# Kernel optimization log

Measured on AMD Instinct MI355X. Metric: run time of the kernel, lower is better.

Reference implementation:

```python
import jax, jax.numpy as jnp
import numpy as np

N_NODES = 100000
N_EDGES = 1600000
IN_C, HID_C, OUT_C = 128, 128, 64


def setup_inputs() -> dict:
    key = jax.random.key(0)
    ks = jax.random.split(key, 9)
    features = jax.random.normal(ks[0], (N_NODES, IN_C), dtype=jnp.float32)
    src = jax.random.randint(ks[1], (N_EDGES,), 0, N_NODES, dtype=jnp.int32)
    dst = jax.random.randint(ks[2], (N_EDGES,), 0, N_NODES, dtype=jnp.int32)
    def glorot(k, fan_in, fan_out):
        lim = float(np.sqrt(6.0 / (fan_in + fan_out)))
        return jax.random.uniform(k, (fan_in, fan_out), jnp.float32, -lim, lim)
    return {
        "features": features, "src": src, "dst": dst,
        "W1": glorot(ks[3], IN_C, HID_C), "b1": jnp.zeros((HID_C,), jnp.float32),
        "W2": glorot(ks[4], HID_C, HID_C), "b2": jnp.zeros((HID_C,), jnp.float32),
        "W3": glorot(ks[5], HID_C, OUT_C), "b3": jnp.zeros((OUT_C,), jnp.float32),
    }


def _graph_conv(x, src, dst, W, b, inv_sqrt_out, inv_sqrt_in):
    # DGL GraphConv, norm='both': h = D_in^{-1/2} A D_out^{-1/2} (x W) + b
    h = (x * inv_sqrt_out[:, None]) @ W            # [N, out]
    agg = jax.ops.segment_sum(h[src], dst, num_segments=N_NODES)
    return agg * inv_sqrt_in[:, None] + b


def reference(features, src, dst, W1, b1, W2, b2, W3, b3):
    ones = jnp.ones((N_EDGES,), jnp.float32)
    deg_out = jnp.clip(jax.ops.segment_sum(ones, src, num_segments=N_NODES), 1.0)
    deg_in = jnp.clip(jax.ops.segment_sum(ones, dst, num_segments=N_NODES), 1.0)
    iso, isi = deg_out ** -0.5, deg_in ** -0.5
    x = jax.nn.relu(_graph_conv(features, src, dst, W1, b1, iso, isi))
    x = jax.nn.relu(_graph_conv(x, src, dst, W2, b2, iso, isi))
    x = _graph_conv(x, src, dst, W3, b3, iso, isi)
    return jax.nn.log_softmax(x, axis=1)
```

## Files before the change

kernel.cpp:

```cpp
#include <hip/hip_runtime.h>
#include <hip/hip_bf16.h>

#define IN_C 128
#define HID_C 128
#define OUT_C 64

typedef unsigned short u16;
typedef unsigned int   u32;
typedef __attribute__((ext_vector_type(8))) short short8;
typedef __attribute__((ext_vector_type(4))) float f32x4;
typedef __attribute__((ext_vector_type(2))) float f32x2;

__device__ __forceinline__ u16 bf16_bits(float x) {
    __hip_bfloat16 h = __float2bfloat16(x);
    return *(u16*)&h;
}
__device__ __forceinline__ void split_hi_lo(float a, u16& hi, u16& lo) {
    __hip_bfloat16 h = __float2bfloat16(a);
    float hf = __bfloat162float(h);
    __hip_bfloat16 l = __float2bfloat16(a - hf);
    hi = *(u16*)&h; lo = *(u16*)&l;
}
__device__ __forceinline__ void pk_acc(f32x2& acc, u32 v) {
    f32x2 val;
    val.x = __uint_as_float(v << 16);
    val.y = __uint_as_float(v & 0xffff0000u);
    asm("v_pk_add_f32 %0, %0, %1" : "+v"(acc) : "v"(val));
}


__global__ __launch_bounds__(256)
void part_hist2(const int* __restrict__ src, const int* __restrict__ dst,
                int* __restrict__ bh, int E, int K, int NB) {
    const int b = blockIdx.x;
    extern __shared__ int lh[];
    for (int i = threadIdx.x; i < 2 * K; i += 256) lh[i] = 0;
    __syncthreads();
    const int lo = (int)((long long)E * b / NB);
    const int hi = (int)((long long)E * (b + 1) / NB);
    for (int i = lo + threadIdx.x; i < hi; i += 256) {
        int d = __builtin_nontemporal_load(&dst[i]);
        int s = __builtin_nontemporal_load(&src[i]);
        atomicAdd(&lh[d >> 8], 1);
        atomicAdd(&lh[K + (s >> 8)], 1);
    }
    __syncthreads();
    for (int k = threadIdx.x; k < K; k += 256) {
        bh[k * NB + b]            = lh[k];
        bh[(K + k) * NB + b]      = lh[K + k];
    }
}

__global__ __launch_bounds__(256)
void part_scatter2(const int* __restrict__ src, const int* __restrict__ dst,
                   const int* __restrict__ ofs, u32* __restrict__ pairs,
                   int E, int K, int NB) {
    const int b = blockIdx.x;
    extern __shared__ int lcur[];
    for (int k = threadIdx.x; k < 2 * K; k += 256) lcur[k] = ofs[k * NB + b];
    __syncthreads();
    const int lo = (int)((long long)E * b / NB);
    const int hi = (int)((long long)E * (b + 1) / NB);
    for (int i = lo + threadIdx.x; i < hi; i += 256) {
        int d = __builtin_nontemporal_load(&dst[i]);
        int s = __builtin_nontemporal_load(&src[i]);
        int p1 = atomicAdd(&lcur[d >> 8], 1);
        pairs[p1] = ((u32)s << 8) | (u32)(d & 255);
        int p2 = atomicAdd(&lcur[K + (s >> 8)], 1);
        pairs[p2] = (u32)s;
    }
}

__global__ __launch_bounds__(256)
void bucket_count2(const u32* __restrict__ pairs, const int* __restrict__ OFS,
                   int* __restrict__ cnt_in, int* __restrict__ cnt_out,
                   int N, int NB, int K, int E) {
    const int kk = blockIdx.x;
    const bool is_src = kk >= K;
    const int k = is_src ? kk - K : kk;
    const int* ofs = OFS + (is_src ? K * NB : 0);
    int* cnt = is_src ? cnt_out : cnt_in;
    const int cap = is_src ? 2 * E : E;
    __shared__ int lc[256];
    lc[threadIdx.x] = 0;
    __syncthreads();
    const int s0 = ofs[k * NB];
    const int s1 = (k == K - 1) ? cap : ofs[(k + 1) * NB];
    for (int i = s0 + threadIdx.x; i < s1; i += 256)
        atomicAdd(&lc[pairs[i] & 255], 1);
    __syncthreads();
    const int node = k * 256 + threadIdx.x;
    if (node < N) cnt[node] = lc[threadIdx.x];
}

__global__ __launch_bounds__(256)
void bucket_fill(const u32* __restrict__ pairs, const int* __restrict__ ofs,
                 const int* __restrict__ row_start, int* __restrict__ csr,
                 int N, int NB, int K, int E) {
    const int k = blockIdx.x;
    __shared__ int lcur[256];
    const int node = k * 256 + threadIdx.x;
    lcur[threadIdx.x] = (node < N) ? row_start[node] : 0;
    __syncthreads();
    const int s0 = ofs[k * NB];
    const int s1 = (k == K - 1) ? E : ofs[(k + 1) * NB];
    for (int i = s0 + threadIdx.x; i < s1; i += 256) {
        u32 pr = pairs[i];
        int p = atomicAdd(&lcur[pr & 255], 1);
        csr[p] = (int)(pr >> 8);
    }
    __syncthreads();
    if (node < N) {
        int end = row_start[node + 1];
        for (int q = lcur[threadIdx.x]; q < end; ++q) csr[q] = N;
    }
}


__global__ __launch_bounds__(256)
void scan_pass1(const int* __restrict__ in, int* __restrict__ blocksum, int M) {
    const int b = blockIdx.x, t = threadIdx.x;
    const int base = b * 1024 + t * 4;
    int s = 0;
#pragma unroll
    for (int j = 0; j < 4; ++j) {
        int idx = base + j;
        if (idx < M) s += in[idx];
    }
#pragma unroll
    for (int off = 32; off >= 1; off >>= 1) s += __shfl_xor(s, off);
    __shared__ int wsum[4];
    if ((t & 63) == 0) wsum[t >> 6] = s;
    __syncthreads();
    if (t == 0) blocksum[b] = wsum[0] + wsum[1] + wsum[2] + wsum[3];
}

__global__ __launch_bounds__(256)
void scan_pass1p(const int* __restrict__ in, int* __restrict__ blocksum, int M) {
    const int b = blockIdx.x, t = threadIdx.x;
    const int base = b * 1024 + t * 4;
    int s = 0;
#pragma unroll
    for (int j = 0; j < 4; ++j) {
        int idx = base + j;
        if (idx < M) s += (in[idx] + 3) & ~3;
    }
#pragma unroll
    for (int off = 32; off >= 1; off >>= 1) s += __shfl_xor(s, off);
    __shared__ int wsum[4];
    if ((t & 63) == 0) wsum[t >> 6] = s;
    __syncthreads();
    if (t == 0) blocksum[b] = wsum[0] + wsum[1] + wsum[2] + wsum[3];
}

__global__ __launch_bounds__(1024)
void scan_g2(int* __restrict__ a, int nb) {
    __shared__ int s[1024];
    const int t = threadIdx.x;
    int v = (t < nb) ? a[t] : 0;
    s[t] = v;
    __syncthreads();
    for (int off = 1; off < 1024; off <<= 1) {
        int x = (t >= off) ? s[t - off] : 0;
        __syncthreads();
        s[t] += x;
        __syncthreads();
    }
    if (t < nb) a[t] = s[t] - v;
}

__global__ __launch_bounds__(256)
void scan_g3(const int* __restrict__ in, const int* __restrict__ blockoff,
             int* __restrict__ out, int M) {
    __shared__ int ssum[256];
    const int b = blockIdx.x, t = threadIdx.x;
    const int base = b * 1024 + t * 4;
    int c[4];
#pragma unroll
    for (int j = 0; j < 4; ++j) {
        int idx = base + j;
        c[j] = (idx < M) ? in[idx] : 0;
    }
    const int tot = c[0] + c[1] + c[2] + c[3];
    ssum[t] = tot;
    __syncthreads();
    for (int off = 1; off < 256; off <<= 1) {
        int v = (t >= off) ? ssum[t - off] : 0;
        __syncthreads();
        ssum[t] += v;
        __syncthreads();
    }
    int run = blockoff[b] + ssum[t] - tot;
#pragma unroll
    for (int j = 0; j < 4; ++j) {
        int idx = base + j;
        if (idx < M) { out[idx] = run; run += c[j]; }
    }
}

__global__ __launch_bounds__(256)
void scan_pass3n(const int* __restrict__ cnt_in, const int* __restrict__ cnt_out,
                 const int* __restrict__ blockoff, int* __restrict__ row_start,
                 float* __restrict__ iso, float* __restrict__ isi, int N) {
    __shared__ int ssum[256];
    const int b = blockIdx.x, t = threadIdx.x;
    const int base = b * 1024 + t * 4;
    int c[4];
#pragma unroll
    for (int j = 0; j < 4; ++j) {
        int idx = base + j;
        c[j] = (idx < N) ? cnt_in[idx] : 0;
    }
    const int tot = ((c[0] + 3) & ~3) + ((c[1] + 3) & ~3) + ((c[2] + 3) & ~3) + ((c[3] + 3) & ~3);
    ssum[t] = tot;
    __syncthreads();
    for (int off = 1; off < 256; off <<= 1) {
        int v = (t >= off) ? ssum[t - off] : 0;
        __syncthreads();
        ssum[t] += v;
        __syncthreads();
    }
    int run = blockoff[b] + ssum[t] - tot;
#pragma unroll
    for (int j = 0; j < 4; ++j) {
        int idx = base + j;
        if (idx < N) {
            row_start[idx] = run;
            run += (c[j] + 3) & ~3;
            int di = c[j] < 1 ? 1 : c[j];
            int co = cnt_out[idx];
            int dd = co < 1 ? 1 : co;
            isi[idx] = rsqrtf((float)di);
            iso[idx] = rsqrtf((float)dd);
            if (idx == N - 1) row_start[N] = run;
        }
    }
}


__global__ __launch_bounds__(128)
void wt_prep_all(const float* __restrict__ W1, const float* __restrict__ W2,
                 const float* __restrict__ W3, u16* __restrict__ Wt1,
                 u16* __restrict__ Wt2, u16* __restrict__ Wt3) {
    const int b = blockIdx.x, k = threadIdx.x;
    if (b < 128)       Wt1[b * 128 + k] = bf16_bits(W1[k * 128 + b]);
    else if (b < 256)  { int c = b - 128; Wt2[c * 128 + k] = bf16_bits(W2[k * 128 + c]); }
    else               { int c = b - 256; Wt3[c * 128 + k] = bf16_bits(W3[k * 64 + c]); }
}


template <int C>
__device__ __forceinline__
void mfma_store2(const u16* sAh, const u16* sAl, const u16* __restrict__ Wt,
                 u16* __restrict__ H, int row0, int N, int t) {
    constexpr int NT = C / 16;
    const int wid = t >> 6, lane = t & 63;
    const int r0 = wid * 16;
    const int arow = r0 + (lane & 15);
    const int kb = (lane >> 4) * 8;

    f32x4 acc[NT];
#pragma unroll
    for (int i = 0; i < NT; ++i) acc[i] = (f32x4){0.f, 0.f, 0.f, 0.f};

    const u16* wbase = Wt + (size_t)(lane & 15) * 128 + kb;

#pragma unroll
    for (int kk = 0; kk < 4; ++kk) {
        short8 ah = *(const short8*)(&sAh[arow * 136 + kk * 32 + kb]);
        short8 al = *(const short8*)(&sAl[arow * 136 + kk * 32 + kb]);
#pragma unroll
        for (int ct = 0; ct < NT; ++ct) {
            short8 bf = *(const short8*)(wbase + ct * 16 * 128 + kk * 32);
            acc[ct] = __builtin_amdgcn_mfma_f32_16x16x32_bf16(ah, bf, acc[ct], 0, 0, 0);
            acc[ct] = __builtin_amdgcn_mfma_f32_16x16x32_bf16(al, bf, acc[ct], 0, 0, 0);
        }
    }

    const int rbase = row0 + r0 + (lane >> 4) * 4;
#pragma unroll
    for (int ct = 0; ct < NT; ++ct) {
        int gcol = ct * 16 + (lane & 15);
#pragma unroll
        for (int r = 0; r < 4; ++r) {
            int grow = rbase + r;
            if (grow < N) H[(size_t)grow * C + gcol] = bf16_bits(acc[ct][r]);
        }
    }
}

template <int C>
__device__ __forceinline__
void mfma_store1(const u16* sA, const u16* __restrict__ Wt,
                 u16* __restrict__ H, int row0, int N, int t) {
    constexpr int NT = C / 16;
    const int wid = t >> 6, lane = t & 63;
    const int r0 = wid * 16;
    const int arow = r0 + (lane & 15);
    const int kb = (lane >> 4) * 8;

    f32x4 acc[NT];
#pragma unroll
    for (int i = 0; i < NT; ++i) acc[i] = (f32x4){0.f, 0.f, 0.f, 0.f};

    const u16* wbase = Wt + (size_t)(lane & 15) * 128 + kb;

#pragma unroll
    for (int kk = 0; kk < 4; ++kk) {
        short8 a = *(const short8*)(&sA[arow * 136 + kk * 32 + kb]);
#pragma unroll
        for (int ct = 0; ct < NT; ++ct) {
            short8 bf = *(const short8*)(wbase + ct * 16 * 128 + kk * 32);
            acc[ct] = __builtin_amdgcn_mfma_f32_16x16x32_bf16(a, bf, acc[ct], 0, 0, 0);
        }
    }

    const int rbase = row0 + r0 + (lane >> 4) * 4;
#pragma unroll
    for (int ct = 0; ct < NT; ++ct) {
        int gcol = ct * 16 + (lane & 15);
#pragma unroll
        for (int r = 0; r < 4; ++r) {
            int grow = rbase + r;
            if (grow < N) H[(size_t)grow * C + gcol] = bf16_bits(acc[ct][r]);
        }
    }
}


__global__ __launch_bounds__(256)
void gemm1_fused(const float* __restrict__ X, const float* __restrict__ iso,
                 const u16* __restrict__ Wt, u16* __restrict__ H, int N) {
    __shared__ u16 sAh[64 * 136];
    __shared__ u16 sAl[64 * 136];
    const int t = threadIdx.x;
    const int row0 = blockIdx.x * 64;

    if (blockIdx.x == 0 && t < 64) ((u32*)H)[(size_t)N * 64 + t] = 0;

    for (int i = t; i < 2048; i += 256) {
        int r = i >> 5, kv = (i & 31) << 2;
        int gr = row0 + r;
        if (gr >= N) gr = N - 1;
        float s = iso[gr];
        float4 x = *(const float4*)(X + (size_t)gr * 128 + kv);
        u16 h0, l0, h1, l1, h2, l2, h3, l3;
        split_hi_lo(x.x * s, h0, l0);
        split_hi_lo(x.y * s, h1, l1);
        split_hi_lo(x.z * s, h2, l2);
        split_hi_lo(x.w * s, h3, l3);
        uint2 hp = make_uint2((u32)h0 | ((u32)h1 << 16), (u32)h2 | ((u32)h3 << 16));
        uint2 lp = make_uint2((u32)l0 | ((u32)l1 << 16), (u32)l2 | ((u32)l3 << 16));
        *(uint2*)(&sAh[r * 136 + kv]) = hp;
        *(uint2*)(&sAl[r * 136 + kv]) = lp;
    }
    __syncthreads();
    mfma_store2<128>(sAh, sAl, Wt, H, row0, N, t);
}


template <int C>
__global__ __launch_bounds__(256)
void gemm_mfma(const u16* __restrict__ A,
               const u16* __restrict__ Wt, u16* __restrict__ H, int N) {
    __shared__ u16 sA[64 * 136];
    const int t = threadIdx.x;
    const int row0 = blockIdx.x * 64;

    if (blockIdx.x == 0 && t < C / 2) ((u32*)H)[(size_t)N * (C / 2) + t] = 0;

    for (int c = t; c < 1024; c += 256) {
        int r = c >> 4, kc = c & 15;
        int gr = row0 + r;
        if (gr >= N) gr = N - 1;
        *(uint4*)(&sA[r * 136 + kc * 8]) = *(const uint4*)(A + (size_t)gr * 128 + kc * 8);
    }
    __syncthreads();
    mfma_store1<C>(sA, Wt, H, row0, N, t);
}


__device__ __forceinline__
void gather128w(const u16* __restrict__ Hin, const int* __restrict__ csr,
                int rs, int re, int lane, f32x2* acc) {
    const int sub = lane >> 4;
    const int cb  = (lane & 15) * 8;
    int e = rs;
    while (e < re) {
        int nloc = re - e;
        if (nloc > 64) nloc = 64;
        int idx = (lane < nloc) ? __builtin_nontemporal_load(&csr[e + lane]) : 0;
        int j = 0;
        for (; j + 16 <= nloc; j += 16) {
            int r0 = __shfl(idx, j + sub);
            int r1 = __shfl(idx, j + 4 + sub);
            int r2 = __shfl(idx, j + 8 + sub);
            int r3 = __shfl(idx, j + 12 + sub);
            uint4 v0 = *(const uint4*)(Hin + (size_t)r0 * 128 + cb);
            uint4 v1 = *(const uint4*)(Hin + (size_t)r1 * 128 + cb);
            uint4 v2 = *(const uint4*)(Hin + (size_t)r2 * 128 + cb);
            uint4 v3 = *(const uint4*)(Hin + (size_t)r3 * 128 + cb);
            pk_acc(acc[0], v0.x); pk_acc(acc[1], v0.y); pk_acc(acc[2], v0.z); pk_acc(acc[3], v0.w);
            pk_acc(acc[0], v1.x); pk_acc(acc[1], v1.y); pk_acc(acc[2], v1.z); pk_acc(acc[3], v1.w);
            pk_acc(acc[0], v2.x); pk_acc(acc[1], v2.y); pk_acc(acc[2], v2.z); pk_acc(acc[3], v2.w);
            pk_acc(acc[0], v3.x); pk_acc(acc[1], v3.y); pk_acc(acc[2], v3.z); pk_acc(acc[3], v3.w);
        }
        for (; j < nloc; j += 4) {
            int r0 = __shfl(idx, j + sub);
            uint4 v0 = *(const uint4*)(Hin + (size_t)r0 * 128 + cb);
            pk_acc(acc[0], v0.x); pk_acc(acc[1], v0.y); pk_acc(acc[2], v0.z); pk_acc(acc[3], v0.w);
        }
        e += nloc;
    }
}


__global__ __launch_bounds__(256)
void agg_relu(const u16* __restrict__ H, const int* __restrict__ row_start,
              const int* __restrict__ csr_src, const float* __restrict__ isi,
              const float* __restrict__ iso, const float* __restrict__ bias,
              u16* __restrict__ A, int N) {
    const int wid  = (int)((blockIdx.x * (size_t)blockDim.x + threadIdx.x) >> 6);
    const int lane = threadIdx.x & 63;
    if (wid >= N) return;
    const int rs = row_start[wid];
    const int re = row_start[wid + 1];

    f32x2 acc[4];
#pragma unroll
    for (int i = 0; i < 4; ++i) { acc[i].x = 0.f; acc[i].y = 0.f; }
    gather128w(H, csr_src, rs, re, lane, acc);

#pragma unroll
    for (int i = 0; i < 4; ++i) {
        acc[i].x += __shfl_xor(acc[i].x, 16); acc[i].y += __shfl_xor(acc[i].y, 16);
        acc[i].x += __shfl_xor(acc[i].x, 32); acc[i].y += __shfl_xor(acc[i].y, 32);
    }

    if (lane < 16) {
        const float sc = isi[wid], so = iso[wid];
        float4 ba = *(const float4*)(bias + lane * 8);
        float4 bb = *(const float4*)(bias + lane * 8 + 4);
        float o[8];
        o[0] = acc[0].x * sc + ba.x; o[1] = acc[0].y * sc + ba.y;
        o[2] = acc[1].x * sc + ba.z; o[3] = acc[1].y * sc + ba.w;
        o[4] = acc[2].x * sc + bb.x; o[5] = acc[2].y * sc + bb.y;
        o[6] = acc[3].x * sc + bb.z; o[7] = acc[3].y * sc + bb.w;
        u32 hp[4];
#pragma unroll
        for (int i = 0; i < 4; ++i) {
            u16 h0 = bf16_bits(fmaxf(o[2 * i], 0.f) * so);
            u16 h1 = bf16_bits(fmaxf(o[2 * i + 1], 0.f) * so);
            hp[i] = (u32)h0 | ((u32)h1 << 16);
        }
        *(uint4*)(A + (size_t)wid * 128 + lane * 8) = *(uint4*)hp;
    }
}


__global__ __launch_bounds__(256)
void agg_final(const u16* __restrict__ H, const int* __restrict__ row_start,
               const int* __restrict__ csr_src, const float* __restrict__ isi,
               const float* __restrict__ bias, float* __restrict__ Out, int N) {
    const int wid  = (int)((blockIdx.x * (size_t)blockDim.x + threadIdx.x) >> 6);
    const int lane = threadIdx.x & 63;
    if (wid >= N) return;
    const int rs = row_start[wid];
    const int re = row_start[wid + 1];
    const int sub = lane >> 4;
    const int cb  = (lane & 15) * 4;

    f32x2 a0, a1;
    a0.x = a0.y = a1.x = a1.y = 0.f;
    int e = rs;
    while (e < re) {
        int nloc = re - e;
        if (nloc > 64) nloc = 64;
        int idx = (lane < nloc) ? __builtin_nontemporal_load(&csr_src[e + lane]) : 0;
        int j = 0;
        for (; j + 16 <= nloc; j += 16) {
            int r0 = __shfl(idx, j + sub);
            int r1 = __shfl(idx, j + 4 + sub);
            int r2 = __shfl(idx, j + 8 + sub);
            int r3 = __shfl(idx, j + 12 + sub);
            uint2 v0 = *(const uint2*)(H + (size_t)r0 * 64 + cb);
            uint2 v1 = *(const uint2*)(H + (size_t)r1 * 64 + cb);
            uint2 v2 = *(const uint2*)(H + (size_t)r2 * 64 + cb);
            uint2 v3 = *(const uint2*)(H + (size_t)r3 * 64 + cb);
            pk_acc(a0, v0.x); pk_acc(a1, v0.y);
            pk_acc(a0, v1.x); pk_acc(a1, v1.y);
            pk_acc(a0, v2.x); pk_acc(a1, v2.y);
            pk_acc(a0, v3.x); pk_acc(a1, v3.y);
        }
        for (; j < nloc; j += 4) {
            int r0 = __shfl(idx, j + sub);
            uint2 v0 = *(const uint2*)(H + (size_t)r0 * 64 + cb);
            pk_acc(a0, v0.x); pk_acc(a1, v0.y);
        }
        e += nloc;
    }

    a0.x += __shfl_xor(a0.x, 16); a0.y += __shfl_xor(a0.y, 16);
    a0.x += __shfl_xor(a0.x, 32); a0.y += __shfl_xor(a0.y, 32);
    a1.x += __shfl_xor(a1.x, 16); a1.y += __shfl_xor(a1.y, 16);
    a1.x += __shfl_xor(a1.x, 32); a1.y += __shfl_xor(a1.y, 32);

    const float sc = isi[wid];
    float4 b4 = *(const float4*)(bias + (lane & 15) * 4);
    float v0 = a0.x * sc + b4.x;
    float v1 = a0.y * sc + b4.y;
    float v2 = a1.x * sc + b4.z;
    float v3 = a1.y * sc + b4.w;
    float m = fmaxf(fmaxf(v0, v1), fmaxf(v2, v3));
#pragma unroll
    for (int off = 8; off >= 1; off >>= 1) m = fmaxf(m, __shfl_xor(m, off));
    float ss = expf(v0 - m) + expf(v1 - m) + expf(v2 - m) + expf(v3 - m);
#pragma unroll
    for (int off = 8; off >= 1; off >>= 1) ss += __shfl_xor(ss, off);
    float lg = m + logf(ss);
    if (lane < 16) {
        float4 o = make_float4(v0 - lg, v1 - lg, v2 - lg, v3 - lg);
        *(float4*)(Out + (size_t)wid * 64 + lane * 4) = o;
    }
}


extern "C" void kernel_launch(void* const* d_in, const int* in_sizes, int n_in,
                              void* d_out, int out_size, void* d_ws, size_t ws_size,
                              hipStream_t stream) {
    const float* features = (const float*)d_in[0];
    const int*   src      = (const int*)d_in[1];
    const int*   dst      = (const int*)d_in[2];
    const float* W1       = (const float*)d_in[3];
    const float* b1       = (const float*)d_in[4];
    const float* W2       = (const float*)d_in[5];
    const float* b2       = (const float*)d_in[6];
    const float* W3       = (const float*)d_in[7];
    const float* b3       = (const float*)d_in[8];
    float*       out      = (float*)d_out;

    const int N  = in_sizes[0] / IN_C;
    const int E  = in_sizes[1];
    const int K  = (N + 255) >> 8;
    const int NB = 256;
    const int M  = 2 * K * NB;
    const int nbe = (M + 1023) / 1024;
    const int nb  = (N + 1023) / 1024;

    char* ws = (char*)d_ws;
    const size_t SLOT = 400128;
    int*   cnt_out   = (int*)(ws + 0 * SLOT);
    int*   cnt_in    = (int*)(ws + 1 * SLOT);
    int*   row_start = (int*)(ws + 2 * SLOT);
    float* iso       = (float*)(ws + 3 * SLOT);
    float* isi       = (float*)(ws + 4 * SLOT);
    int*   blocksum  = (int*)(ws + 5 * SLOT);
    int*   eblocksum = blocksum + 2048;
    int*   csr       = (int*)(ws + 6 * SLOT);
    char*  p         = ws + 6 * SLOT + 8000000;
    int*   BH        = (int*)p;
    int*   OFS       = (int*)(p + 1000000);
    u32*   pairs     = (u32*)(p + 2000000);
    u16*   Hb        = (u16*)(p + 14800000);
    u16*   Ab        = (u16*)(p + 40500000);
    u16*   Wt1       = (u16*)(p + 66100000);
    u16*   Wt2       = Wt1 + 128 * 128;
    u16*   Wt3       = Wt2 + 128 * 128;

    const size_t ldsK2 = (size_t)(2 * K) * sizeof(int);

    part_hist2<<<NB, 256, ldsK2, stream>>>(src, dst, BH, E, K, NB);
    scan_pass1<<<nbe, 256, 0, stream>>>(BH, eblocksum, M);
    scan_g2<<<1, 1024, 0, stream>>>(eblocksum, nbe);
    scan_g3<<<nbe, 256, 0, stream>>>(BH, eblocksum, OFS, M);
    part_scatter2<<<NB, 256, ldsK2, stream>>>(src, dst, OFS, pairs, E, K, NB);
    bucket_count2<<<2 * K, 256, 0, stream>>>(pairs, OFS, cnt_in, cnt_out, N, NB, K, E);
    scan_pass1p<<<nb, 256, 0, stream>>>(cnt_in, blocksum, N);
    scan_g2<<<1, 1024, 0, stream>>>(blocksum, nb);
    scan_pass3n<<<nb, 256, 0, stream>>>(cnt_in, cnt_out, blocksum, row_start, iso, isi, N);
    bucket_fill<<<K, 256, 0, stream>>>(pairs, OFS, row_start, csr, N, NB, K, E);

    wt_prep_all<<<320, 128, 0, stream>>>(W1, W2, W3, Wt1, Wt2, Wt3);

    const int gblocks = (N + 63) / 64;
    const int ablocks = (int)(((size_t)N * 64 + 255) / 256);

    gemm1_fused<<<gblocks, 256, 0, stream>>>(features, iso, Wt1, Hb, N);
    agg_relu<<<ablocks, 256, 0, stream>>>(Hb, row_start, csr, isi, iso, b1, Ab, N);
    gemm_mfma<128><<<gblocks, 256, 0, stream>>>(Ab, Wt2, Hb, N);
    agg_relu<<<ablocks, 256, 0, stream>>>(Hb, row_start, csr, isi, iso, b2, Ab, N);
    gemm_mfma<64><<<gblocks, 256, 0, stream>>>(Ab, Wt3, Hb, N);
    agg_final<<<ablocks, 256, 0, stream>>>(Hb, row_start, csr, isi, b3, out, N);
}
```

Measured before the change: 358.6 us.

## Compute out-degree via global atomics and fuse per-bucket count, scan and CSR fill

The source-side partition (second histogram and scatter of src pairs) is replaced by a direct global-atomic out-degree count. In-degree counting, the padded row-offset scan, the normalization factors and the CSR fill are merged into one per-bucket kernel. Row offsets now come from the bucket offset plus a per-bucket local scan with padding slack (k*768), so aggregation kernels take an explicit row_end array. This cuts several launches and halves the pair traffic, at the cost of global atomic contention on the out-degree counters and gaps in the CSR layout.

```diff
diff --git a/kernel.cpp b/kernel.cpp
--- a/kernel.cpp
+++ b/kernel.cpp
@@ -29,90 +29,100 @@
 }
 
 
-__global__ __launch_bounds__(256)
-void part_hist2(const int* __restrict__ src, const int* __restrict__ dst,
-                int* __restrict__ bh, int E, int K, int NB) {
+__global__ void zero_kernel(int* __restrict__ p, int n) {
+    int i = blockIdx.x * blockDim.x + threadIdx.x;
+    if (i < n) p[i] = 0;
+}
+
+__global__ void degree_src(const int* __restrict__ src, int* __restrict__ cnt, int E) {
+    for (int i = blockIdx.x * blockDim.x + threadIdx.x; i < E; i += gridDim.x * blockDim.x)
+        atomicAdd(&cnt[src[i]], 1);
+}
+
+
+__global__ __launch_bounds__(256)
+void part_hist(const int* __restrict__ dst, int* __restrict__ bh,
+               int E, int K, int NB) {
     const int b = blockIdx.x;
     extern __shared__ int lh[];
-    for (int i = threadIdx.x; i < 2 * K; i += 256) lh[i] = 0;
+    for (int i = threadIdx.x; i < K; i += 256) lh[i] = 0;
+    __syncthreads();
+    const int lo = (int)((long long)E * b / NB);
+    const int hi = (int)((long long)E * (b + 1) / NB);
+    for (int i = lo + threadIdx.x; i < hi; i += 256)
+        atomicAdd(&lh[__builtin_nontemporal_load(&dst[i]) >> 8], 1);
+    __syncthreads();
+    for (int k = threadIdx.x; k < K; k += 256)
+        bh[k * NB + b] = lh[k];
+}
+
+__global__ __launch_bounds__(256)
+void part_scatter(const int* __restrict__ src, const int* __restrict__ dst,
+                  const int* __restrict__ ofs, u32* __restrict__ pairs,
+                  int E, int K, int NB) {
+    const int b = blockIdx.x;
+    extern __shared__ int lcur[];
+    for (int k = threadIdx.x; k < K; k += 256) lcur[k] = ofs[k * NB + b];
     __syncthreads();
     const int lo = (int)((long long)E * b / NB);
     const int hi = (int)((long long)E * (b + 1) / NB);
     for (int i = lo + threadIdx.x; i < hi; i += 256) {
         int d = __builtin_nontemporal_load(&dst[i]);
         int s = __builtin_nontemporal_load(&src[i]);
-        atomicAdd(&lh[d >> 8], 1);
-        atomicAdd(&lh[K + (s >> 8)], 1);
-    }
-    __syncthreads();
-    for (int k = threadIdx.x; k < K; k += 256) {
-        bh[k * NB + b]            = lh[k];
-        bh[(K + k) * NB + b]      = lh[K + k];
-    }
-}
-
-__global__ __launch_bounds__(256)
-void part_scatter2(const int* __restrict__ src, const int* __restrict__ dst,
-                   const int* __restrict__ ofs, u32* __restrict__ pairs,
-                   int E, int K, int NB) {
-    const int b = blockIdx.x;
-    extern __shared__ int lcur[];
-    for (int k = threadIdx.x; k < 2 * K; k += 256) lcur[k] = ofs[k * NB + b];
-    __syncthreads();
-    const int lo = (int)((long long)E * b / NB);
-    const int hi = (int)((long long)E * (b + 1) / NB);
-    for (int i = lo + threadIdx.x; i < hi; i += 256) {
-        int d = __builtin_nontemporal_load(&dst[i]);
-        int s = __builtin_nontemporal_load(&src[i]);
-        int p1 = atomicAdd(&lcur[d >> 8], 1);
-        pairs[p1] = ((u32)s << 8) | (u32)(d & 255);
-        int p2 = atomicAdd(&lcur[K + (s >> 8)], 1);
-        pairs[p2] = (u32)s;
-    }
-}
-
-__global__ __launch_bounds__(256)
-void bucket_count2(const u32* __restrict__ pairs, const int* __restrict__ OFS,
-                   int* __restrict__ cnt_in, int* __restrict__ cnt_out,
-                   int N, int NB, int K, int E) {
-    const int kk = blockIdx.x;
-    const bool is_src = kk >= K;
-    const int k = is_src ? kk - K : kk;
-    const int* ofs = OFS + (is_src ? K * NB : 0);
-    int* cnt = is_src ? cnt_out : cnt_in;
-    const int cap = is_src ? 2 * E : E;
+        int p = atomicAdd(&lcur[d >> 8], 1);
+        pairs[p] = ((u32)s << 8) | (u32)(d & 255);
+    }
+}
+
+__global__ __launch_bounds__(256)
+void bucket_count_fill(const u32* __restrict__ pairs, const int* __restrict__ OFS,
+                       const int* __restrict__ cnt_out,
+                       int* __restrict__ csr, int* __restrict__ row_start,
+                       int* __restrict__ row_end, float* __restrict__ iso,
+                       float* __restrict__ isi, int N, int NB, int K, int E) {
+    const int k = blockIdx.x, t = threadIdx.x;
     __shared__ int lc[256];
-    lc[threadIdx.x] = 0;
-    __syncthreads();
-    const int s0 = ofs[k * NB];
-    const int s1 = (k == K - 1) ? cap : ofs[(k + 1) * NB];
-    for (int i = s0 + threadIdx.x; i < s1; i += 256)
+    __shared__ int lpre[256];
+    lc[t] = 0;
+    __syncthreads();
+    const int s0 = OFS[k * NB];
+    const int s1 = (k == K - 1) ? E : OFS[(k + 1) * NB];
+    for (int i = s0 + t; i < s1; i += 256)
         atomicAdd(&lc[pairs[i] & 255], 1);
     __syncthreads();
-    const int node = k * 256 + threadIdx.x;
-    if (node < N) cnt[node] = lc[threadIdx.x];
-}
-
-__global__ __launch_bounds__(256)
-void bucket_fill(const u32* __restrict__ pairs, const int* __restrict__ ofs,
-                 const int* __restrict__ row_start, int* __restrict__ csr,
-                 int N, int NB, int K, int E) {
-    const int k = blockIdx.x;
-    __shared__ int lcur[256];
-    const int node = k * 256 + threadIdx.x;
-    lcur[threadIdx.x] = (node < N) ? row_start[node] : 0;
-    __syncthreads();
-    const int s0 = ofs[k * NB];
-    const int s1 = (k == K - 1) ? E : ofs[(k + 1) * NB];
-    for (int i = s0 + threadIdx.x; i < s1; i += 256) {
+    const int c  = lc[t];
+    const int cp = (c + 3) & ~3;
+    lpre[t] = cp;
+    __syncthreads();
+    for (int off = 1; off < 256; off <<= 1) {
+        int v = (t >= off) ? lpre[t - off] : 0;
+        __syncthreads();
+        lpre[t] += v;
+        __syncthreads();
+    }
+    const int start = s0 + k * 768 + lpre[t] - cp;
+    const int myend = start + cp;
+    const int node = k * 256 + t;
+    if (node < N) {
+        row_start[node] = start;
+        row_end[node]   = myend;
+        int di = c < 1 ? 1 : c;
+        int co = cnt_out[node];
+        int dd = co < 1 ? 1 : co;
+        isi[node] = rsqrtf((float)di);
+        iso[node] = rsqrtf((float)dd);
+    }
+    __syncthreads();
+    lc[t] = start;
+    __syncthreads();
+    for (int i = s0 + t; i < s1; i += 256) {
         u32 pr = pairs[i];
-        int p = atomicAdd(&lcur[pr & 255], 1);
+        int p = atomicAdd(&lc[pr & 255], 1);
         csr[p] = (int)(pr >> 8);
     }
     __syncthreads();
     if (node < N) {
-        int end = row_start[node + 1];
-        for (int q = lcur[threadIdx.x]; q < end; ++q) csr[q] = N;
+        for (int q = lc[t]; q < myend; ++q) csr[q] = N;
     }
 }
 
@@ -126,24 +136,6 @@
     for (int j = 0; j < 4; ++j) {
         int idx = base + j;
         if (idx < M) s += in[idx];
-    }
-#pragma unroll
-    for (int off = 32; off >= 1; off >>= 1) s += __shfl_xor(s, off);
-    __shared__ int wsum[4];
-    if ((t & 63) == 0) wsum[t >> 6] = s;
-    __syncthreads();
-    if (t == 0) blocksum[b] = wsum[0] + wsum[1] + wsum[2] + wsum[3];
-}
-
-__global__ __launch_bounds__(256)
-void scan_pass1p(const int* __restrict__ in, int* __restrict__ blocksum, int M) {
-    const int b = blockIdx.x, t = threadIdx.x;
-    const int base = b * 1024 + t * 4;
-    int s = 0;
-#pragma unroll
-    for (int j = 0; j < 4; ++j) {
-        int idx = base + j;
-        if (idx < M) s += (in[idx] + 3) & ~3;
     }
 #pragma unroll
     for (int off = 32; off >= 1; off >>= 1) s += __shfl_xor(s, off);
@@ -195,45 +187,6 @@
     for (int j = 0; j < 4; ++j) {
         int idx = base + j;
         if (idx < M) { out[idx] = run; run += c[j]; }
-    }
-}
-
-__global__ __launch_bounds__(256)
-void scan_pass3n(const int* __restrict__ cnt_in, const int* __restrict__ cnt_out,
-                 const int* __restrict__ blockoff, int* __restrict__ row_start,
-                 float* __restrict__ iso, float* __restrict__ isi, int N) {
-    __shared__ int ssum[256];
-    const int b = blockIdx.x, t = threadIdx.x;
-    const int base = b * 1024 + t * 4;
-    int c[4];
-#pragma unroll
-    for (int j = 0; j < 4; ++j) {
-        int idx = base + j;
-        c[j] = (idx < N) ? cnt_in[idx] : 0;
-    }
-    const int tot = ((c[0] + 3) & ~3) + ((c[1] + 3) & ~3) + ((c[2] + 3) & ~3) + ((c[3] + 3) & ~3);
-    ssum[t] = tot;
-    __syncthreads();
-    for (int off = 1; off < 256; off <<= 1) {
-        int v = (t >= off) ? ssum[t - off] : 0;
-        __syncthreads();
-        ssum[t] += v;
-        __syncthreads();
-    }
-    int run = blockoff[b] + ssum[t] - tot;
-#pragma unroll
-    for (int j = 0; j < 4; ++j) {
-        int idx = base + j;
-        if (idx < N) {
-            row_start[idx] = run;
-            run += (c[j] + 3) & ~3;
-            int di = c[j] < 1 ? 1 : c[j];
-            int co = cnt_out[idx];
-            int dd = co < 1 ? 1 : co;
-            isi[idx] = rsqrtf((float)di);
-            iso[idx] = rsqrtf((float)dd);
-            if (idx == N - 1) row_start[N] = run;
-        }
     }
 }
 
@@ -417,6 +370,7 @@
 
 __global__ __launch_bounds__(256)
 void agg_relu(const u16* __restrict__ H, const int* __restrict__ row_start,
+              const int* __restrict__ row_end,
               const int* __restrict__ csr_src, const float* __restrict__ isi,
               const float* __restrict__ iso, const float* __restrict__ bias,
               u16* __restrict__ A, int N) {
@@ -424,7 +378,7 @@
     const int lane = threadIdx.x & 63;
     if (wid >= N) return;
     const int rs = row_start[wid];
-    const int re = row_start[wid + 1];
+    const int re = row_end[wid];
 
     f32x2 acc[4];
 #pragma unroll
@@ -460,13 +414,14 @@
 
 __global__ __launch_bounds__(256)
 void agg_final(const u16* __restrict__ H, const int* __restrict__ row_start,
+               const int* __restrict__ row_end,
                const int* __restrict__ csr_src, const float* __restrict__ isi,
                const float* __restrict__ bias, float* __restrict__ Out, int N) {
     const int wid  = (int)((blockIdx.x * (size_t)blockDim.x + threadIdx.x) >> 6);
     const int lane = threadIdx.x & 63;
     if (wid >= N) return;
     const int rs = row_start[wid];
-    const int re = row_start[wid + 1];
+    const int re = row_end[wid];
     const int sub = lane >> 4;
     const int cb  = (lane & 15) * 4;
 
@@ -543,42 +498,39 @@
     const int E  = in_sizes[1];
     const int K  = (N + 255) >> 8;
     const int NB = 256;
-    const int M  = 2 * K * NB;
+    const int M  = K * NB;
     const int nbe = (M + 1023) / 1024;
-    const int nb  = (N + 1023) / 1024;
 
     char* ws = (char*)d_ws;
     const size_t SLOT = 400128;
     int*   cnt_out   = (int*)(ws + 0 * SLOT);
-    int*   cnt_in    = (int*)(ws + 1 * SLOT);
+    int*   row_end   = (int*)(ws + 1 * SLOT);
     int*   row_start = (int*)(ws + 2 * SLOT);
     float* iso       = (float*)(ws + 3 * SLOT);
     float* isi       = (float*)(ws + 4 * SLOT);
-    int*   blocksum  = (int*)(ws + 5 * SLOT);
-    int*   eblocksum = blocksum + 2048;
+    int*   eblocksum = (int*)(ws + 5 * SLOT);
     int*   csr       = (int*)(ws + 6 * SLOT);
     char*  p         = ws + 6 * SLOT + 8000000;
     int*   BH        = (int*)p;
-    int*   OFS       = (int*)(p + 1000000);
-    u32*   pairs     = (u32*)(p + 2000000);
-    u16*   Hb        = (u16*)(p + 14800000);
-    u16*   Ab        = (u16*)(p + 40500000);
-    u16*   Wt1       = (u16*)(p + 66100000);
+    int*   OFS       = (int*)(p + 500000);
+    u32*   pairs     = (u32*)(p + 1000000);
+    u16*   Hb        = (u16*)(p + 7400000);
+    u16*   Ab        = (u16*)(p + 33100000);
+    u16*   Wt1       = (u16*)(p + 58700000);
     u16*   Wt2       = Wt1 + 128 * 128;
     u16*   Wt3       = Wt2 + 128 * 128;
 
-    const size_t ldsK2 = (size_t)(2 * K) * sizeof(int);
-
-    part_hist2<<<NB, 256, ldsK2, stream>>>(src, dst, BH, E, K, NB);
+    const size_t ldsK = (size_t)K * sizeof(int);
+
+    zero_kernel<<<(N + 255) / 256, 256, 0, stream>>>(cnt_out, N);
+    degree_src<<<1024, 256, 0, stream>>>(src, cnt_out, E);
+    part_hist<<<NB, 256, ldsK, stream>>>(dst, BH, E, K, NB);
     scan_pass1<<<nbe, 256, 0, stream>>>(BH, eblocksum, M);
     scan_g2<<<1, 1024, 0, stream>>>(eblocksum, nbe);
     scan_g3<<<nbe, 256, 0, stream>>>(BH, eblocksum, OFS, M);
-    part_scatter2<<<NB, 256, ldsK2, stream>>>(src, dst, OFS, pairs, E, K, NB);
-    bucket_count2<<<2 * K, 256, 0, stream>>>(pairs, OFS, cnt_in, cnt_out, N, NB, K, E);
-    scan_pass1p<<<nb, 256, 0, stream>>>(cnt_in, blocksum, N);
-    scan_g2<<<1, 1024, 0, stream>>>(blocksum, nb);
-    scan_pass3n<<<nb, 256, 0, stream>>>(cnt_in, cnt_out, blocksum, row_start, iso, isi, N);
-    bucket_fill<<<K, 256, 0, stream>>>(pairs, OFS, row_start, csr, N, NB, K, E);
+    part_scatter<<<NB, 256, ldsK, stream>>>(src, dst, OFS, pairs, E, K, NB);
+    bucket_count_fill<<<K, 256, 0, stream>>>(pairs, OFS, cnt_out, csr, row_start,
+                                             row_end, iso, isi, N, NB, K, E);
 
     wt_prep_all<<<320, 128, 0, stream>>>(W1, W2, W3, Wt1, Wt2, Wt3);
 
@@ -586,9 +538,9 @@
     const int ablocks = (int)(((size_t)N * 64 + 255) / 256);
 
     gemm1_fused<<<gblocks, 256, 0, stream>>>(features, iso, Wt1, Hb, N);
-    agg_relu<<<ablocks, 256, 0, stream>>>(Hb, row_start, csr, isi, iso, b1, Ab, N);
+    agg_relu<<<ablocks, 256, 0, stream>>>(Hb, row_start, row_end, csr, isi, iso, b1, Ab, N);
     gemm_mfma<128><<<gblocks, 256, 0, stream>>>(Ab, Wt2, Hb, N);
-    agg_relu<<<ablocks, 256, 0, stream>>>(Hb, row_start, csr, isi, iso, b2, Ab, N);
+    agg_relu<<<ablocks, 256, 0, stream>>>(Hb, row_start, row_end, csr, isi, iso, b2, Ab, N);
     gemm_mfma<64><<<gblocks, 256, 0, stream>>>(Ab, Wt3, Hb, N);
-    agg_final<<<ablocks, 256, 0, stream>>>(Hb, row_start, csr, isi, b3, out, N);
-}
+    agg_final<<<ablocks, 256, 0, stream>>>(Hb, row_start, row_end, csr, isi, b3, out, N);
+}
```

After: 434.2 us. +21.1%, slower.
